# Performance work log

Measured on AMD Instinct MI355X. Metric: run time of the kernel, lower is better.

The kernel has to match this reference:

```python
import jax, jax.numpy as jnp
import numpy as np


def setup_inputs() -> dict:
    key = jax.random.key(0)
    ks = jax.random.split(key, 6)
    B, T, S, E, D = 8, 128, 512, 512, 512  # batch, trg_len, src_len, enc_dim, trg_dim
    W_SCALE = 0.03  # small init to keep tanh unsaturated
    return {
        "hidden": jax.random.normal(ks[0], (B, T, D), jnp.float32),
        "encoder_outputs": jax.random.normal(ks[1], (B, S, E), jnp.float32),
        "encoder_mask": jnp.ones((B, S), jnp.float32),
        "W_attn": jax.random.normal(ks[2], (D, E + D), jnp.float32) * W_SCALE,
        "b_attn": jnp.zeros((D,), jnp.float32),
        "W_v": jax.random.normal(ks[3], (1, D), jnp.float32) * W_SCALE,
        "b_v": jnp.zeros((1,), jnp.float32),
        "W_out": jax.random.normal(ks[4], (D, E + D), jnp.float32) * W_SCALE,
    }


def masked_softmax(x, m, axis=-1):
    # faithful to repo: x*m, stable exp, e*m, normalize with eps
    x = x * m
    e_x = jnp.exp(x - jnp.max(x, axis=axis, keepdims=True))
    e_x = e_x * m
    return e_x / (jnp.sum(e_x, axis=axis, keepdims=True) + 1e-6)


def reference(hidden, encoder_outputs, encoder_mask, W_attn, b_attn, W_v, b_v, W_out):
    B, T, D = hidden.shape
    S = encoder_outputs.shape[1]
    # concat order in get_energy is (hidden_i, encoder_outputs), so split W_attn
    W_h = W_attn[:, :D]   # (D_out, trg_dim)
    W_e = W_attn[:, D:]   # (D_out, enc_dim)
    # Linear(concat) == h@W_h^T + e@W_e^T + b; vectorized over all (t, s) pairs
    hp = jnp.einsum('btd,kd->btk', hidden, W_h)            # (B,T,K)
    ep = jnp.einsum('bse,ke->bsk', encoder_outputs, W_e)   # (B,S,K)
    feat = jnp.tanh(hp[:, :, None, :] + ep[:, None, :, :] + b_attn)  # (B,T,S,K)
    energies = jnp.einsum('btsk,k->bts', feat, W_v[0]) + b_v[0]      # (B,T,S)
    # forward: energies * mask, then masked softmax
    m = encoder_mask[:, None, :]  # (B,1,S)
    energies = energies * m
    attn_weights = masked_softmax(energies, m, axis=-1)    # (B,T,S)
    weighted_context = jnp.einsum('bts,bse->bte', attn_weights, encoder_outputs)
    h_cat = jnp.concatenate([weighted_context, hidden], axis=-1)  # (B,T,E+D)
    h_tilde = jnp.tanh(jnp.einsum('btc,dc->btd', h_cat, W_out))   # (B,T,D)
    return h_tilde, weighted_context, attn_weights
```

## Files before the change

### kernel.cpp

```cpp
#include <hip/hip_runtime.h>
#include <hip/hip_bf16.h>
#include <math.h>

typedef unsigned short u16;
typedef unsigned int u32;
typedef __bf16 bf16x8 __attribute__((ext_vector_type(8)));
typedef float f32x4 __attribute__((ext_vector_type(4)));

#define OUT_WC   524288LL
#define OUT_ATTN 1048576LL
#define C2 2.8853900817779268f
#define LOG2E 1.4426950408889634f
#define LAS 40

__device__ inline u16 f2b(float f) {
    return (u16)((__float_as_uint(f) + 0x8000u) >> 16);
}
__device__ inline u32 pkcvt(float x, float y) {
    __hip_bfloat162 h = __float22bfloat162_rn(make_float2(x, y));
    return *(u32*)&h;
}
__device__ inline float tanh_fast(float x) {
    return 1.f - 2.f * __builtin_amdgcn_rcpf(__builtin_amdgcn_exp2f(C2 * x) + 1.f);
}

__global__ __launch_bounds__(256) void proj(
    const float* __restrict__ hidden, const float* __restrict__ enc,
    const float* __restrict__ Wattn, const float* __restrict__ battn,
    const float* __restrict__ Wout,
    float* __restrict__ hp, u16* __restrict__ ept, float* __restrict__ hh)
{
    __shared__ u16 lA[64 * LAS];
    __shared__ u16 lB[64 * LAS];
    const int tid = threadIdx.x;
    const int wvi = tid >> 6, ln = tid & 63;
    const int wm = wvi >> 1, wn = wvi & 1;
    const int l16 = ln & 15, quad = ln >> 4;
    const int blk = blockIdx.x;
    int bx, by, zz = 0, lda, ldb, mode;
    const float *A, *B;
    if (blk < 512) {
        mode = 0;
        zz = blk >> 6; by = (blk >> 3) & 7; bx = blk & 7;
        A = Wattn + 512; lda = 1024;
        B = enc + (long long)zz * 262144; ldb = 512;
    } else if (blk < 640) {
        mode = 1;
        int i = blk - 512; by = i >> 3; bx = i & 7;
        A = hidden; lda = 512;
        B = Wattn; ldb = 1024;
    } else {
        mode = 2;
        int i = blk - 640; by = i >> 3; bx = i & 7;
        A = hidden; lda = 512;
        B = Wout + 512; ldb = 1024;
    }
    const int m0 = by * 64, n0 = bx * 64;
    const int srow = tid >> 2, skof = (tid & 3) * 8;
    const float* Ap = A + (long long)(m0 + srow) * lda + skof;
    const float* Bp = B + (long long)(n0 + srow) * ldb + skof;

    f32x4 acc00 = {0,0,0,0}, acc01 = {0,0,0,0}, acc10 = {0,0,0,0}, acc11 = {0,0,0,0};

    for (int k0 = 0; k0 < 512; k0 += 32) {
        float4 a0v = *(const float4*)(Ap + k0);
        float4 a1v = *(const float4*)(Ap + k0 + 4);
        float4 b0v = *(const float4*)(Bp + k0);
        float4 b1v = *(const float4*)(Bp + k0 + 4);
        __syncthreads();
        *(uint4*)&lA[srow * LAS + skof] =
            make_uint4(pkcvt(a0v.x,a0v.y), pkcvt(a0v.z,a0v.w), pkcvt(a1v.x,a1v.y), pkcvt(a1v.z,a1v.w));
        *(uint4*)&lB[srow * LAS + skof] =
            make_uint4(pkcvt(b0v.x,b0v.y), pkcvt(b0v.z,b0v.w), pkcvt(b1v.x,b1v.y), pkcvt(b1v.z,b1v.w));
        __syncthreads();
        bf16x8 a0 = *(const bf16x8*)&lA[(wm * 32      + l16) * LAS + quad * 8];
        bf16x8 a1 = *(const bf16x8*)&lA[(wm * 32 + 16 + l16) * LAS + quad * 8];
        bf16x8 b0 = *(const bf16x8*)&lB[(wn * 32      + l16) * LAS + quad * 8];
        bf16x8 b1 = *(const bf16x8*)&lB[(wn * 32 + 16 + l16) * LAS + quad * 8];
        acc00 = __builtin_amdgcn_mfma_f32_16x16x32_bf16(a0, b0, acc00, 0, 0, 0);
        acc01 = __builtin_amdgcn_mfma_f32_16x16x32_bf16(a0, b1, acc01, 0, 0, 0);
        acc10 = __builtin_amdgcn_mfma_f32_16x16x32_bf16(a1, b0, acc10, 0, 0, 0);
        acc11 = __builtin_amdgcn_mfma_f32_16x16x32_bf16(a1, b1, acc11, 0, 0, 0);
    }

    const f32x4* accs[4] = { &acc00, &acc01, &acc10, &acc11 };
    #pragma unroll
    for (int i = 0; i < 2; ++i) {
        #pragma unroll
        for (int j = 0; j < 2; ++j) {
            const f32x4& a = *accs[i * 2 + j];
            #pragma unroll
            for (int r = 0; r < 4; ++r) {
                int m = m0 + wm * 32 + i * 16 + quad * 4 + r;
                int n = n0 + wn * 32 + j * 16 + l16;
                float v = a[r];
                if (mode == 0)
                    ept[(long long)zz * 262144 + (long long)m * 512 + n] =
                        f2b(__builtin_amdgcn_exp2f(C2 * v));
                else if (mode == 1)
                    hp[(long long)m * 512 + n] = C2 * (v + battn[n]);
                else
                    hh[(long long)m * 512 + n] = v;
            }
        }
    }
}

__device__ inline float wred_sum(float v) {
    #pragma unroll
    for (int i = 32; i > 0; i >>= 1) v += __shfl_xor(v, i);
    return v;
}
__device__ inline float bred_sum8(float v, float* red, int tid) {
    v = wred_sum(v);
    __syncthreads();
    if ((tid & 63) == 0) red[tid >> 6] = v;
    __syncthreads();
    float s = 0.f;
    #pragma unroll
    for (int i = 0; i < 8; ++i) s += red[i];
    return s;
}
__device__ inline void bred2_max(float v0, float v1, float* red, int tid,
                                 float* o0, float* o1) {
    #pragma unroll
    for (int i = 32; i > 0; i >>= 1) {
        v0 = fmaxf(v0, __shfl_xor(v0, i));
        v1 = fmaxf(v1, __shfl_xor(v1, i));
    }
    __syncthreads();
    if ((tid & 63) == 0) { red[tid >> 6] = v0; red[8 + (tid >> 6)] = v1; }
    __syncthreads();
    float a0 = red[0], a1 = red[8];
    #pragma unroll
    for (int i = 1; i < 8; ++i) { a0 = fmaxf(a0, red[i]); a1 = fmaxf(a1, red[8 + i]); }
    *o0 = a0; *o1 = a1;
}
__device__ inline void bred2_sum(float v0, float v1, float* red, int tid,
                                 float* o0, float* o1) {
    #pragma unroll
    for (int i = 32; i > 0; i >>= 1) { v0 += __shfl_xor(v0, i); v1 += __shfl_xor(v1, i); }
    __syncthreads();
    if ((tid & 63) == 0) { red[tid >> 6] = v0; red[8 + (tid >> 6)] = v1; }
    __syncthreads();
    float a0 = 0.f, a1 = 0.f;
    #pragma unroll
    for (int i = 0; i < 8; ++i) { a0 += red[i]; a1 += red[8 + i]; }
    *o0 = a0; *o1 = a1;
}

__device__ inline void proc8(uint4 c, float4 hw, float* a0, float* a1) {
    u32 cc[4] = {c.x, c.y, c.z, c.w};
    #pragma unroll
    for (int i = 0; i < 4; ++i) {
        float xl = __uint_as_float(cc[i] << 16);
        float xh = __uint_as_float(cc[i] & 0xFFFF0000u);
        float rl0 = __builtin_amdgcn_rcpf(fmaf(hw.x, xl, 1.f));
        float rh0 = __builtin_amdgcn_rcpf(fmaf(hw.x, xh, 1.f));
        float rl1 = __builtin_amdgcn_rcpf(fmaf(hw.y, xl, 1.f));
        float rh1 = __builtin_amdgcn_rcpf(fmaf(hw.y, xh, 1.f));
        a0[2*i]   = fmaf(hw.z, rl0, a0[2*i]);
        a0[2*i+1] = fmaf(hw.z, rh0, a0[2*i+1]);
        a1[2*i]   = fmaf(hw.z, rl1, a1[2*i]);
        a1[2*i+1] = fmaf(hw.z, rh1, a1[2*i+1]);
    }
}

__global__ __launch_bounds__(512) void energies(
    const float* __restrict__ maskp, const float* __restrict__ hp,
    const u16* __restrict__ ept, const float* __restrict__ Wv,
    const float* __restrict__ bvp, const float* __restrict__ enc,
    float* __restrict__ attn, float* __restrict__ wc)
{
    __shared__ __align__(16) float4 hpw[512];
    __shared__ float pa[2][8][512];
    __shared__ __align__(16) float2 aL[512];
    __shared__ float red[16];
    const int tid = threadIdx.x;
    const int b = blockIdx.x >> 6;
    const int t0 = (blockIdx.x & 63) * 2;

    float w = Wv[tid];
    float h0 = hp[(long long)(b * 128 + t0) * 512 + tid];
    float h1 = hp[(long long)(b * 128 + t0 + 1) * 512 + tid];
    hpw[tid] = make_float4(__builtin_amdgcn_exp2f(h0), __builtin_amdgcn_exp2f(h1), w, 0.f);
    float sumWv = bred_sum8(w, red, tid);

    const int kg = tid >> 6, sl = tid & 63;
    const int s0 = sl * 8;
    const u16* eb = ept + (long long)b * 262144 + (kg * 64) * 512 + s0;
    const float4* hq = &hpw[kg * 64];

    float a0[8] = {0,0,0,0,0,0,0,0}, a1[8] = {0,0,0,0,0,0,0,0};
    uint4 c0 = *(const uint4*)(eb);
    uint4 c1 = *(const uint4*)(eb + 512);
    uint4 c2 = *(const uint4*)(eb + 1024);
    uint4 c3 = *(const uint4*)(eb + 1536);
    for (int kk = 0; kk < 60; kk += 4) {
        const u16* nb = eb + (kk + 4) * 512;
        uint4 n0 = *(const uint4*)(nb);
        uint4 n1 = *(const uint4*)(nb + 512);
        uint4 n2 = *(const uint4*)(nb + 1024);
        uint4 n3 = *(const uint4*)(nb + 1536);
        proc8(c0, hq[kk],     a0, a1);
        proc8(c1, hq[kk + 1], a0, a1);
        proc8(c2, hq[kk + 2], a0, a1);
        proc8(c3, hq[kk + 3], a0, a1);
        c0 = n0; c1 = n1; c2 = n2; c3 = n3;
    }
    proc8(c0, hq[60], a0, a1);
    proc8(c1, hq[61], a0, a1);
    proc8(c2, hq[62], a0, a1);
    proc8(c3, hq[63], a0, a1);

    *(float4*)&pa[0][kg][s0]     = make_float4(a0[0], a0[1], a0[2], a0[3]);
    *(float4*)&pa[0][kg][s0 + 4] = make_float4(a0[4], a0[5], a0[6], a0[7]);
    *(float4*)&pa[1][kg][s0]     = make_float4(a1[0], a1[1], a1[2], a1[3]);
    *(float4*)&pa[1][kg][s0 + 4] = make_float4(a1[4], a1[5], a1[6], a1[7]);
    __syncthreads();

    const int s = tid;
    float A0 = 0.f, A1 = 0.f;
    #pragma unroll
    for (int g = 0; g < 8; ++g) { A0 += pa[0][g][s]; A1 += pa[1][g][s]; }
    float mv = maskp[(long long)b * 512 + s];
    float bv0 = bvp[0];
    float r0 = (bv0 + sumWv - 2.f * A0) * mv; r0 *= mv;
    float r1 = (bv0 + sumWv - 2.f * A1) * mv; r1 *= mv;

    float mx0, mx1;
    bred2_max(r0, r1, red, tid, &mx0, &mx1);
    float ex0 = __builtin_amdgcn_exp2f((r0 - mx0) * LOG2E) * mv;
    float ex1 = __builtin_amdgcn_exp2f((r1 - mx1) * LOG2E) * mv;
    float sm0, sm1;
    bred2_sum(ex0, ex1, red, tid, &sm0, &sm1);
    float at0 = ex0 * (1.f / (sm0 + 1e-6f));
    float at1 = ex1 * (1.f / (sm1 + 1e-6f));
    attn[(long long)(b * 128 + t0) * 512 + s]     = at0;
    attn[(long long)(b * 128 + t0 + 1) * 512 + s] = at1;
    aL[s] = make_float2(at0, at1);
    __syncthreads();

    const float* encb = enc + (long long)b * 262144 + tid;
    const float4* aL4 = (const float4*)aL;
    float acc0 = 0.f, acc1 = 0.f;
    for (int ss = 0; ss < 512; ss += 8) {
        float ev[8];
        #pragma unroll
        for (int i = 0; i < 8; ++i) ev[i] = encb[(ss + i) * 512];
        #pragma unroll
        for (int i = 0; i < 4; ++i) {
            float4 ap = aL4[(ss >> 1) + i];
            acc0 = fmaf(ap.x, ev[2*i],   acc0);
            acc1 = fmaf(ap.y, ev[2*i],   acc1);
            acc0 = fmaf(ap.z, ev[2*i+1], acc0);
            acc1 = fmaf(ap.w, ev[2*i+1], acc1);
        }
    }
    wc[(long long)(b * 128 + t0) * 512 + tid]     = acc0;
    wc[(long long)(b * 128 + t0 + 1) * 512 + tid] = acc1;
}

__global__ __launch_bounds__(256) void hout_k(
    const float* __restrict__ wc, const float* __restrict__ Wout,
    const float* __restrict__ hh, float* __restrict__ out)
{
    __shared__ u16 lA[32 * LAS];
    __shared__ u16 lB[64 * LAS];
    const int tid = threadIdx.x;
    const int wvi = tid >> 6, ln = tid & 63;
    const int l16 = ln & 15, quad = ln >> 4;
    const int msub = wvi & 1, npair = wvi >> 1;
    const int m0 = blockIdx.y * 32, n0 = blockIdx.x * 64;
    const int rowA = tid >> 3, kofA = (tid & 7) * 4;
    const int rowB = tid >> 2, kofB = (tid & 3) * 8;
    f32x4 acc0 = {0,0,0,0}, acc1 = {0,0,0,0};

    for (int k0 = 0; k0 < 512; k0 += 32) {
        float4 av = *(const float4*)(wc + (long long)(m0 + rowA) * 512 + k0 + kofA);
        const float* Bp = Wout + (long long)(n0 + rowB) * 1024 + k0 + kofB;
        float4 bv0 = *(const float4*)Bp;
        float4 bv1 = *(const float4*)(Bp + 4);
        __syncthreads();
        *(uint2*)&lA[rowA * LAS + kofA] = make_uint2(pkcvt(av.x, av.y), pkcvt(av.z, av.w));
        int kk = kofB ^ (((rowB >> 3) & 3) << 3);
        *(uint4*)&lB[rowB * LAS + kk] =
            make_uint4(pkcvt(bv0.x,bv0.y), pkcvt(bv0.z,bv0.w), pkcvt(bv1.x,bv1.y), pkcvt(bv1.z,bv1.w));
        __syncthreads();
        bf16x8 a = *(const bf16x8*)&lA[(msub * 16 + l16) * LAS + quad * 8];
        int nr0 = npair * 32 + l16, nr1 = nr0 + 16;
        bf16x8 b0 = *(const bf16x8*)&lB[nr0 * LAS + (quad * 8 ^ (((nr0 >> 3) & 3) << 3))];
        bf16x8 b1 = *(const bf16x8*)&lB[nr1 * LAS + (quad * 8 ^ (((nr1 >> 3) & 3) << 3))];
        acc0 = __builtin_amdgcn_mfma_f32_16x16x32_bf16(a, b0, acc0, 0, 0, 0);
        acc1 = __builtin_amdgcn_mfma_f32_16x16x32_bf16(a, b1, acc1, 0, 0, 0);
    }
    #pragma unroll
    for (int j = 0; j < 2; ++j) {
        const f32x4& a = j ? acc1 : acc0;
        #pragma unroll
        for (int r = 0; r < 4; ++r) {
            int m = m0 + msub * 16 + quad * 4 + r;
            int n = n0 + npair * 32 + j * 16 + l16;
            long long idx = (long long)m * 512 + n;
            out[idx] = tanh_fast(a[r] + hh[idx]);
        }
    }
}

extern "C" void kernel_launch(void* const* d_in, const int* in_sizes, int n_in,
                              void* d_out, int out_size, void* d_ws, size_t ws_size,
                              hipStream_t stream)
{
    const float* hidden = (const float*)d_in[0];
    const float* enc    = (const float*)d_in[1];
    const float* mask   = (const float*)d_in[2];
    const float* Wattn  = (const float*)d_in[3];
    const float* battn  = (const float*)d_in[4];
    const float* Wv     = (const float*)d_in[5];
    const float* bvp    = (const float*)d_in[6];
    const float* Wout   = (const float*)d_in[7];
    float* out = (float*)d_out;

    float* hp  = (float*)d_ws;
    u16*   ept = (u16*)((char*)d_ws + (2 << 20));
    float* hh  = (float*)((char*)d_ws + (6 << 20));

    proj<<<768, 256, 0, stream>>>(hidden, enc, Wattn, battn, Wout, hp, ept, hh);
    energies<<<512, 512, 0, stream>>>(mask, hp, ept, Wv, bvp, enc,
                                      out + OUT_ATTN, out + OUT_WC);
    hout_k<<<dim3(8, 32, 1), 256, 0, stream>>>(out + OUT_WC, Wout, hh, out);
}
```

Before: 149.3 us.

## Pre-convert inputs to bf16 once and stage hidden projection in output buffer

Adds a conversion kernel that casts enc, hidden, W_attn and W_out to bf16 into workspace once. The projection GEMMs, the context reduction in energies and the output GEMM then load half-width bf16 data with no per-tile conversion. The hidden@W_out partial is written straight into the output buffer, and hout_k reads it back from there instead of from a separate workspace array. This costs an extra launch and an extra full pass over inputs. The context sum now uses bf16-rounded encoder values, which lowers its accuracy.

Measured after the change: 148.9 us. About the same (-0.3%).

```diff
diff --git a/kernel.cpp b/kernel.cpp
--- a/kernel.cpp
+++ b/kernel.cpp
@@ -16,6 +16,7 @@
 __device__ inline u16 f2b(float f) {
     return (u16)((__float_as_uint(f) + 0x8000u) >> 16);
 }
+__device__ inline float b2f(u16 v) { return __uint_as_float(((u32)v) << 16); }
 __device__ inline u32 pkcvt(float x, float y) {
     __hip_bfloat162 h = __float22bfloat162_rn(make_float2(x, y));
     return *(u32*)&h;
@@ -24,10 +25,27 @@
     return 1.f - 2.f * __builtin_amdgcn_rcpf(__builtin_amdgcn_exp2f(C2 * x) + 1.f);
 }
 
+__global__ __launch_bounds__(256) void tobf(
+    const float* __restrict__ enc, const float* __restrict__ hidden,
+    const float* __restrict__ Wattn, const float* __restrict__ Wout,
+    u16* __restrict__ dst)
+{
+    long long i = ((long long)blockIdx.x * 256 + threadIdx.x) * 8;
+    const float* src; long long off;
+    if (i < 2097152)      { src = enc;    off = i; }
+    else if (i < 2621440) { src = hidden; off = i - 2097152; }
+    else if (i < 3145728) { src = Wattn;  off = i - 2621440; }
+    else                  { src = Wout;   off = i - 3145728; }
+    float4 v0 = *(const float4*)(src + off);
+    float4 v1 = *(const float4*)(src + off + 4);
+    *(uint4*)(dst + i) = make_uint4(pkcvt(v0.x, v0.y), pkcvt(v0.z, v0.w),
+                                    pkcvt(v1.x, v1.y), pkcvt(v1.z, v1.w));
+}
+
 __global__ __launch_bounds__(256) void proj(
-    const float* __restrict__ hidden, const float* __restrict__ enc,
-    const float* __restrict__ Wattn, const float* __restrict__ battn,
-    const float* __restrict__ Wout,
+    const u16* __restrict__ hidden_bf, const u16* __restrict__ enc_bf,
+    const u16* __restrict__ Wattn_bf, const float* __restrict__ battn,
+    const u16* __restrict__ Wout_bf,
     float* __restrict__ hp, u16* __restrict__ ept, float* __restrict__ hh)
 {
     __shared__ u16 lA[64 * LAS];
@@ -38,40 +56,36 @@
     const int l16 = ln & 15, quad = ln >> 4;
     const int blk = blockIdx.x;
     int bx, by, zz = 0, lda, ldb, mode;
-    const float *A, *B;
+    const u16 *A, *B;
     if (blk < 512) {
         mode = 0;
         zz = blk >> 6; by = (blk >> 3) & 7; bx = blk & 7;
-        A = Wattn + 512; lda = 1024;
-        B = enc + (long long)zz * 262144; ldb = 512;
+        A = Wattn_bf + 512; lda = 1024;
+        B = enc_bf + (long long)zz * 262144; ldb = 512;
     } else if (blk < 640) {
         mode = 1;
         int i = blk - 512; by = i >> 3; bx = i & 7;
-        A = hidden; lda = 512;
-        B = Wattn; ldb = 1024;
+        A = hidden_bf; lda = 512;
+        B = Wattn_bf; ldb = 1024;
     } else {
         mode = 2;
         int i = blk - 640; by = i >> 3; bx = i & 7;
-        A = hidden; lda = 512;
-        B = Wout + 512; ldb = 1024;
+        A = hidden_bf; lda = 512;
+        B = Wout_bf + 512; ldb = 1024;
     }
     const int m0 = by * 64, n0 = bx * 64;
     const int srow = tid >> 2, skof = (tid & 3) * 8;
-    const float* Ap = A + (long long)(m0 + srow) * lda + skof;
-    const float* Bp = B + (long long)(n0 + srow) * ldb + skof;
+    const u16* Ap = A + (long long)(m0 + srow) * lda + skof;
+    const u16* Bp = B + (long long)(n0 + srow) * ldb + skof;
 
     f32x4 acc00 = {0,0,0,0}, acc01 = {0,0,0,0}, acc10 = {0,0,0,0}, acc11 = {0,0,0,0};
 
     for (int k0 = 0; k0 < 512; k0 += 32) {
-        float4 a0v = *(const float4*)(Ap + k0);
-        float4 a1v = *(const float4*)(Ap + k0 + 4);
-        float4 b0v = *(const float4*)(Bp + k0);
-        float4 b1v = *(const float4*)(Bp + k0 + 4);
+        uint4 av = *(const uint4*)(Ap + k0);
+        uint4 bv = *(const uint4*)(Bp + k0);
         __syncthreads();
-        *(uint4*)&lA[srow * LAS + skof] =
-            make_uint4(pkcvt(a0v.x,a0v.y), pkcvt(a0v.z,a0v.w), pkcvt(a1v.x,a1v.y), pkcvt(a1v.z,a1v.w));
-        *(uint4*)&lB[srow * LAS + skof] =
-            make_uint4(pkcvt(b0v.x,b0v.y), pkcvt(b0v.z,b0v.w), pkcvt(b1v.x,b1v.y), pkcvt(b1v.z,b1v.w));
+        *(uint4*)&lA[srow * LAS + skof] = av;
+        *(uint4*)&lB[srow * LAS + skof] = bv;
         __syncthreads();
         bf16x8 a0 = *(const bf16x8*)&lA[(wm * 32      + l16) * LAS + quad * 8];
         bf16x8 a1 = *(const bf16x8*)&lA[(wm * 32 + 16 + l16) * LAS + quad * 8];
@@ -169,7 +183,7 @@
 __global__ __launch_bounds__(512) void energies(
     const float* __restrict__ maskp, const float* __restrict__ hp,
     const u16* __restrict__ ept, const float* __restrict__ Wv,
-    const float* __restrict__ bvp, const float* __restrict__ enc,
+    const float* __restrict__ bvp, const u16* __restrict__ enc_bf,
     float* __restrict__ attn, float* __restrict__ wc)
 {
     __shared__ __align__(16) float4 hpw[512];
@@ -241,13 +255,13 @@
     aL[s] = make_float2(at0, at1);
     __syncthreads();
 
-    const float* encb = enc + (long long)b * 262144 + tid;
+    const u16* encb = enc_bf + (long long)b * 262144 + tid;
     const float4* aL4 = (const float4*)aL;
     float acc0 = 0.f, acc1 = 0.f;
     for (int ss = 0; ss < 512; ss += 8) {
         float ev[8];
         #pragma unroll
-        for (int i = 0; i < 8; ++i) ev[i] = encb[(ss + i) * 512];
+        for (int i = 0; i < 8; ++i) ev[i] = b2f(encb[(ss + i) * 512]);
         #pragma unroll
         for (int i = 0; i < 4; ++i) {
             float4 ap = aL4[(ss >> 1) + i];
@@ -262,8 +276,8 @@
 }
 
 __global__ __launch_bounds__(256) void hout_k(
-    const float* __restrict__ wc, const float* __restrict__ Wout,
-    const float* __restrict__ hh, float* __restrict__ out)
+    const float* __restrict__ wc, const u16* __restrict__ Wout_bf,
+    float* __restrict__ out)
 {
     __shared__ u16 lA[32 * LAS];
     __shared__ u16 lB[64 * LAS];
@@ -278,14 +292,11 @@
 
     for (int k0 = 0; k0 < 512; k0 += 32) {
         float4 av = *(const float4*)(wc + (long long)(m0 + rowA) * 512 + k0 + kofA);
-        const float* Bp = Wout + (long long)(n0 + rowB) * 1024 + k0 + kofB;
-        float4 bv0 = *(const float4*)Bp;
-        float4 bv1 = *(const float4*)(Bp + 4);
+        uint4 bv = *(const uint4*)(Wout_bf + (long long)(n0 + rowB) * 1024 + k0 + kofB);
         __syncthreads();
         *(uint2*)&lA[rowA * LAS + kofA] = make_uint2(pkcvt(av.x, av.y), pkcvt(av.z, av.w));
         int kk = kofB ^ (((rowB >> 3) & 3) << 3);
-        *(uint4*)&lB[rowB * LAS + kk] =
-            make_uint4(pkcvt(bv0.x,bv0.y), pkcvt(bv0.z,bv0.w), pkcvt(bv1.x,bv1.y), pkcvt(bv1.z,bv1.w));
+        *(uint4*)&lB[rowB * LAS + kk] = bv;
         __syncthreads();
         bf16x8 a = *(const bf16x8*)&lA[(msub * 16 + l16) * LAS + quad * 8];
         int nr0 = npair * 32 + l16, nr1 = nr0 + 16;
@@ -302,7 +313,7 @@
             int m = m0 + msub * 16 + quad * 4 + r;
             int n = n0 + npair * 32 + j * 16 + l16;
             long long idx = (long long)m * 512 + n;
-            out[idx] = tanh_fast(a[r] + hh[idx]);
+            out[idx] = tanh_fast(a[r] + out[idx]);
         }
     }
 }
@@ -323,10 +334,16 @@
 
     float* hp  = (float*)d_ws;
     u16*   ept = (u16*)((char*)d_ws + (2 << 20));
-    float* hh  = (float*)((char*)d_ws + (6 << 20));
-
-    proj<<<768, 256, 0, stream>>>(hidden, enc, Wattn, battn, Wout, hp, ept, hh);
-    energies<<<512, 512, 0, stream>>>(mask, hp, ept, Wv, bvp, enc,
+    u16*   bfp = (u16*)((char*)d_ws + (6 << 20));
+    u16* enc_bf    = bfp;
+    u16* hidden_bf = bfp + 2097152;
+    u16* Wattn_bf  = bfp + 2621440;
+    u16* Wout_bf   = bfp + 3145728;
+
+    tobf<<<1792, 256, 0, stream>>>(enc, hidden, Wattn, Wout, bfp);
+    proj<<<768, 256, 0, stream>>>(hidden_bf, enc_bf, Wattn_bf, battn, Wout_bf,
+                                  hp, ept, out );
+    energies<<<512, 512, 0, stream>>>(mask, hp, ept, Wv, bvp, enc_bf,
                                       out + OUT_ATTN, out + OUT_WC);
-    hout_k<<<dim3(8, 32, 1), 256, 0, stream>>>(out + OUT_WC, Wout, hh, out);
-}
+    hout_k<<<dim3(8, 32, 1), 256, 0, stream>>>(out + OUT_WC, Wout_bf, out);
+}
```
